# Performance work log

Measured on AMD Instinct MI355X. Metric: run time of the kernel, lower is better.

## Reference

```python
import jax, jax.numpy as jnp
import numpy as np

NN_SIZE = 10  # __init__ default nn_size


def setup_inputs() -> dict:
    key = jax.random.key(0)
    k1, k2 = jax.random.split(key)
    B, N, C = 8, 4096, 3
    xyz1 = jax.random.normal(k1, (B, N, C), dtype=jnp.float32)
    # xyz2 is a small deformation of xyz1 (realistic: deformed shape, same topology)
    xyz2 = xyz1 + 0.05 * jax.random.normal(k2, (B, N, C), dtype=jnp.float32)
    return {"xyz1": xyz1, "xyz2": xyz2}


def _knn_idx(pts, k):
    # brute-force squared-euclidean KNN of pts to itself; pts: (B,N,3) -> idx (B,N,k)
    sq = jnp.sum(pts * pts, axis=-1)                             # (B,N)
    d = sq[:, :, None] - 2.0 * jnp.einsum('bnc,bmc->bnm', pts, pts) + sq[:, None, :]
    _, idx = jax.lax.top_k(-d, k)                                # smallest distances
    return idx


def _point_to_plane(xyz, idx, k):
    # gather neighbors, center, PCA normal from 10x3 SVD, signed point-to-plane dist
    B, N, C = xyz.shape
    grouped = jax.vmap(lambda p, i: p[i])(xyz, idx)              # (B,N,k,3)
    center = jnp.mean(grouped, axis=2, keepdims=True)            # (B,N,1,3)
    local = (grouped - center).reshape(B * N, k, C)              # (B*N,k,3)
    _, _, vh = jnp.linalg.svd(local, full_matrices=False)        # vh: (B*N,3,3)
    # torch V[:, :, -1] == row -1 of Vh: singular vector of smallest singular value
    normals = jax.lax.stop_gradient(vh[:, -1, :].reshape(B, N, C))
    return jnp.sum((xyz - center[:, :, 0, :]) * normals, axis=-1)  # (B,N)


def reference(xyz1, xyz2):
    idx = _knn_idx(xyz1, NN_SIZE)
    ptof1 = _point_to_plane(xyz1, idx, NN_SIZE)
    ptof2 = _point_to_plane(xyz2, idx, NN_SIZE)
    mse = lambda a, b: jnp.mean((a - b) ** 2)
    loss = mse(jnp.abs(ptof1), jnp.abs(ptof2))
    bent = jnp.maximum(ptof2 - ptof1, 0.0)
    loss = loss + 5.0 * mse(bent, jnp.zeros_like(bent))
    return loss
```

## Files before the change

kernel.cpp:

```cpp
#include <hip/hip_runtime.h>
#include <math.h>

#define BB   8
#define NN   4096
#define KK   10
#define TPB  256
#define NPTS (BB * NN)

#define GPP  16
#define PPB  (TPB / GPP)
#define BPBK (NN / PPB)
#define KNBLK (BB * BPBK)
#define TILE 512
#define CAP  48

#define SVDBLK 256
#define SBLK   256

#define LARTG_OLD 0
#define EPSV  5.9604644775390625e-8
#define UNFLV 1.1754943508222875e-38
#define TOLV (10.0 * EPSV)

static __device__ __forceinline__ double lapy2d(double x, double y) {
  double xa = fabs(x), ya = fabs(y);
  double w = fmax(xa, ya), z = fmin(xa, ya);
  if (z == 0.0) return w;
  double q = z / w;
  return w * sqrt(1.0 + q * q);
}

static __device__ __forceinline__ void lartg(double f, double g,
                                             double &c, double &s, double &r) {
#if LARTG_OLD
  if (g == 0.0) { c = 1.0; s = 0.0; r = f; }
  else if (f == 0.0) { c = 0.0; s = 1.0; r = g; }
  else {
    double d = sqrt(f * f + g * g);
    c = f / d; s = g / d; r = d;
    if (fabs(f) > fabs(g) && c < 0.0) { c = -c; s = -s; r = -r; }
  }
#else
  if (g == 0.0) { c = 1.0; s = 0.0; r = f; }
  else if (f == 0.0) { c = 0.0; s = copysign(1.0, g); r = fabs(g); }
  else {
    double d = sqrt(f * f + g * g);
    c = fabs(f) / d;
    r = copysign(d, f);
    s = g / r;
  }
#endif
}

static __device__ void las2(double f, double g, double h, double &ssmin, double &ssmax) {
  double fa = fabs(f), ga = fabs(g), ha = fabs(h);
  double fhmn = fmin(fa, ha), fhmx = fmax(fa, ha);
  if (fhmn == 0.0) {
    ssmin = 0.0;
    if (fhmx == 0.0) ssmax = ga;
    else {
      double mn = fmin(fhmx, ga), mx = fmax(fhmx, ga);
      double rr = mn / mx;
      ssmax = mx * sqrt(1.0 + rr * rr);
    }
  } else {
    if (ga < fhmx) {
      double as_ = 1.0 + fhmn / fhmx;
      double at  = (fhmx - fhmn) / fhmx;
      double au  = (ga / fhmx); au = au * au;
      double c   = 2.0 / (sqrt(as_ * as_ + au) + sqrt(at * at + au));
      ssmin = fhmn * c;
      ssmax = fhmx / c;
    } else {
      double au = fhmx / ga;
      if (au == 0.0) { ssmin = (fhmn * fhmx) / ga; ssmax = ga; }
      else {
        double as_ = 1.0 + fhmn / fhmx;
        double at  = (fhmx - fhmn) / fhmx;
        double t1 = as_ * au, t2 = at * au;
        double c = 1.0 / (sqrt(1.0 + t1 * t1) + sqrt(1.0 + t2 * t2));
        ssmin = (fhmn * c) * au; ssmin = ssmin + ssmin;
        ssmax = ga / (c + c);
      }
    }
  }
}

static __device__ void lasv2(double f, double g, double h,
                             double &ssmin, double &ssmax,
                             double &snr, double &csr, double &snl, double &csl) {
  double ft = f, fa = fabs(f), ht = h, ha = fabs(h);
  int pmax = 1;
  bool swp = (ha > fa);
  if (swp) { pmax = 3; double t = ft; ft = ht; ht = t; t = fa; fa = ha; ha = t; }
  double gt = g, ga = fabs(g);
  double clt = 0, crt = 0, slt = 0, srt = 0;
  if (ga == 0.0) {
    ssmin = ha; ssmax = fa;
    clt = 1.0; crt = 1.0; slt = 0.0; srt = 0.0;
  } else {
    bool gasmal = true;
    if (ga > fa) {
      pmax = 2;
      if ((fa / ga) < EPSV) {
        gasmal = false;
        ssmax = ga;
        if (ha > 1.0) ssmin = fa / (ga / ha);
        else          ssmin = (fa / ga) * ha;
        clt = 1.0; slt = ht / gt; srt = 1.0; crt = ft / gt;
      }
    }
    if (gasmal) {
      double dd = fa - ha, l;
      if (dd == fa) l = 1.0; else l = dd / fa;
      double mv = gt / ft;
      double t = 2.0 - l;
      double mm = mv * mv, tt = t * t;
      double s = sqrt(tt + mm);
      double r = (l == 0.0) ? fabs(mv) : sqrt(l * l + mm);
      double a = 0.5 * (s + r);
      ssmin = ha / a;
      ssmax = fa * a;
      if (mm == 0.0) {
        if (l == 0.0) t = copysign(2.0, ft) * copysign(1.0, gt);
        else          t = gt / copysign(dd, ft) + mv / t;
      } else {
        t = (mv / (s + t) + mv / (r + l)) * (1.0 + a);
      }
      double lq = sqrt(t * t + 4.0);
      crt = 2.0 / lq;
      srt = t / lq;
      clt = (crt + srt * mv) / a;
      slt = (ht / ft) * srt / a;
    }
  }
  if (swp) { csl = srt; snl = crt; csr = slt; snr = clt; }
  else     { csl = clt; snl = slt; csr = crt; snr = srt; }
  double tsign = 1.0;
  if (pmax == 1) tsign = copysign(1.0, csr) * copysign(1.0, csl) * copysign(1.0, f);
  if (pmax == 2) tsign = copysign(1.0, snr) * copysign(1.0, csl) * copysign(1.0, g);
  if (pmax == 3) tsign = copysign(1.0, snr) * copysign(1.0, snl) * copysign(1.0, h);
  ssmax = copysign(ssmax, tsign);
  ssmin = copysign(ssmin, tsign * copysign(1.0, f) * copysign(1.0, h));
}

static __device__ __forceinline__ void rot_rows(double vt[3][3], int lo, double c, double s) {
  if (c != 1.0 || s != 0.0) {
    for (int k = 0; k < 3; ++k) {
      double tp = vt[lo + 1][k];
      vt[lo + 1][k] = c * tp - s * vt[lo][k];
      vt[lo][k]     = s * tp + c * vt[lo][k];
    }
  }
}

static __device__ void bdsqr3(double d[3], double e[2], double vt[3][3]) {
  const double tol = TOLV;
  double sminoa = fabs(d[0]);
  if (sminoa != 0.0) {
    double mu = sminoa;
    mu = fabs(d[1]) * (mu / (mu + fabs(e[0])));
    sminoa = fmin(sminoa, mu);
    if (sminoa != 0.0) {
      mu = fabs(d[2]) * (mu / (mu + fabs(e[1])));
      sminoa = fmin(sminoa, mu);
    }
  }
  sminoa /= sqrt(3.0);
  double thresh = fmax(tol * sminoa, 54.0 * UNFLV);
  int m = 3, oldll = -1, oldm = -1, idir = 0;
  double sminl = 0.0;
  for (int guard = 0; guard < 500 && m > 1; ++guard) {
    double smax = fabs(d[m - 1]);
    int ll = 0;
    bool split = false;
    for (int lll = 1; lll <= m - 1; ++lll) {
      int l = m - lll;
      double abss = fabs(d[l - 1]);
      double abse = fabs(e[l - 1]);
      if (abse <= thresh) { ll = l; split = true; break; }
      smax = fmax(smax, fmax(abss, abse));
    }
    if (split) {
      e[ll - 1] = 0.0;
      if (ll == m - 1) { m = m - 1; continue; }
      ll = ll + 1;
    } else ll = 1;
    if (ll == m - 1) {
      double sigmn, sigmx, sinr, cosr, sinl, cosl;
      lasv2(d[m - 2], e[m - 2], d[m - 1], sigmn, sigmx, sinr, cosr, sinl, cosl);
      d[m - 2] = sigmx; e[m - 2] = 0.0; d[m - 1] = sigmn;
      for (int k = 0; k < 3; ++k) {
        double x = vt[m - 2][k], y = vt[m - 1][k];
        vt[m - 2][k] = cosr * x + sinr * y;
        vt[m - 1][k] = cosr * y - sinr * x;
      }
      m -= 2;
      continue;
    }
    if (ll > oldm || m < oldll)
      idir = (fabs(d[ll - 1]) >= fabs(d[m - 1])) ? 1 : 2;
    bool deflated = false;
    if (idir == 1) {
      if (fabs(e[m - 2]) <= tol * fabs(d[m - 1])) { e[m - 2] = 0.0; continue; }
      double mu = fabs(d[ll - 1]);
      sminl = mu;
      for (int lll = ll; lll <= m - 1; ++lll) {
        if (fabs(e[lll - 1]) <= tol * mu) { e[lll - 1] = 0.0; deflated = true; break; }
        mu = fabs(d[lll]) * (mu / (mu + fabs(e[lll - 1])));
        sminl = fmin(sminl, mu);
      }
    } else {
      if (fabs(e[ll - 1]) <= tol * fabs(d[ll - 1])) { e[ll - 1] = 0.0; continue; }
      double mu = fabs(d[m - 1]);
      sminl = mu;
      for (int lll = m - 1; lll >= ll; --lll) {
        if (fabs(e[lll - 1]) <= tol * mu) { e[lll - 1] = 0.0; deflated = true; break; }
        mu = fabs(d[lll - 1]) * (mu / (mu + fabs(e[lll - 1])));
        sminl = fmin(sminl, mu);
      }
    }
    if (deflated) continue;
    oldll = ll; oldm = m;
    double shift = 0.0, rdum = 0.0;
    if (!(3.0 * tol * (sminl / smax) <= fmax(EPSV, 0.01 * tol))) {
      double sll;
      if (idir == 1) { sll = fabs(d[ll - 1]); las2(d[m - 2], e[m - 2], d[m - 1], shift, rdum); }
      else           { sll = fabs(d[m - 1]); las2(d[ll - 1], e[ll - 1], d[ll], shift, rdum); }
      if (sll > 0.0 && (shift / sll) * (shift / sll) < EPSV) shift = 0.0;
    }
    double csv[2], snv[2];
    if (shift == 0.0) {
      if (idir == 1) {
        double cs = 1.0, oldcs = 1.0, sn = 0.0, oldsn = 0.0, r = 0.0;
        for (int i = ll; i <= m - 1; ++i) {
          lartg(d[i - 1] * cs, e[i - 1], cs, sn, r);
          if (i > ll) e[i - 2] = oldsn * r;
          lartg(oldcs * r, d[i] * sn, oldcs, oldsn, d[i - 1]);
          csv[i - ll] = cs; snv[i - ll] = sn;
        }
        double h = d[m - 1] * cs;
        d[m - 1] = h * oldcs;
        e[m - 2] = h * oldsn;
        for (int j = 0; j <= m - ll - 1; ++j) rot_rows(vt, ll - 1 + j, csv[j], snv[j]);
        if (fabs(e[m - 2]) <= thresh) e[m - 2] = 0.0;
      } else {
        double cs = 1.0, oldcs = 1.0, sn = 0.0, oldsn = 0.0, r = 0.0;
        for (int i = m; i >= ll + 1; --i) {
          lartg(d[i - 1] * cs, e[i - 2], cs, sn, r);
          if (i < m) e[i - 1] = oldsn * r;
          lartg(oldcs * r, d[i - 2] * sn, oldcs, oldsn, d[i - 1]);
          csv[i - ll - 1] = oldcs; snv[i - ll - 1] = -oldsn;
        }
        double h = d[ll - 1] * cs;
        d[ll - 1] = h * oldcs;
        e[ll - 1] = h * oldsn;
        for (int j = m - ll - 1; j >= 0; --j) rot_rows(vt, ll - 1 + j, csv[j], snv[j]);
        if (fabs(e[ll - 1]) <= thresh) e[ll - 1] = 0.0;
      }
    } else {
      if (idir == 1) {
        double f = (fabs(d[ll - 1]) - shift) * (copysign(1.0, d[ll - 1]) + shift / d[ll - 1]);
        double g = e[ll - 1], cosr, sinr, cosl, sinl, r;
        for (int i = ll; i <= m - 1; ++i) {
          lartg(f, g, cosr, sinr, r);
          if (i > ll) e[i - 2] = r;
          f = cosr * d[i - 1] + sinr * e[i - 1];
          e[i - 1] = cosr * e[i - 1] - sinr * d[i - 1];
          g = sinr * d[i];
          d[i] = cosr * d[i];
          lartg(f, g, cosl, sinl, r);
          d[i - 1] = r;
          f = cosl * e[i - 1] + sinl * d[i];
          d[i] = cosl * d[i] - sinl * e[i - 1];
          if (i < m - 1) { g = sinl * e[i]; e[i] = cosl * e[i]; }
          csv[i - ll] = cosr; snv[i - ll] = sinr;
        }
        e[m - 2] = f;
        for (int j = 0; j <= m - ll - 1; ++j) rot_rows(vt, ll - 1 + j, csv[j], snv[j]);
        if (fabs(e[m - 2]) <= thresh) e[m - 2] = 0.0;
      } else {
        double f = (fabs(d[m - 1]) - shift) * (copysign(1.0, d[m - 1]) + shift / d[m - 1]);
        double g = e[m - 2], cosr, sinr, cosl, sinl, r;
        for (int i = m; i >= ll + 1; --i) {
          lartg(f, g, cosr, sinr, r);
          if (i < m) e[i - 1] = r;
          f = cosr * d[i - 1] + sinr * e[i - 2];
          e[i - 2] = cosr * e[i - 2] - sinr * d[i - 1];
          g = sinr * d[i - 2];
          d[i - 2] = cosr * d[i - 2];
          lartg(f, g, cosl, sinl, r);
          d[i - 1] = r;
          f = cosl * e[i - 2] + sinl * d[i - 2];
          d[i - 2] = cosl * d[i - 2] - sinl * e[i - 2];
          if (i > ll + 1) { g = sinl * e[i - 3]; e[i - 3] = cosl * e[i - 3]; }
          csv[i - ll - 1] = cosr; snv[i - ll - 1] = sinr;
        }
        e[ll - 1] = f;
        for (int j = m - ll - 1; j >= 0; --j) rot_rows(vt, ll - 1 + j, csv[j], snv[j]);
        if (fabs(e[ll - 1]) <= thresh) e[ll - 1] = 0.0;
      }
    }
  }
  for (int i = 0; i < 3; ++i)
    if (d[i] < 0.0) { d[i] = -d[i]; for (int k = 0; k < 3; ++k) vt[i][k] = -vt[i][k]; }
}

static __device__ void lapack_normal(double A[KK][3], double &nx, double &ny, double &nz) {
#pragma unroll
  for (int i = 0; i < 3; ++i) {
    double ss = 0.0;
#pragma unroll
    for (int j = i + 1; j < KK; ++j) ss += A[j][i] * A[j][i];
    double xnorm = sqrt(ss);
    if (xnorm != 0.0) {
      double alpha = A[i][i];
      double beta = -copysign(lapy2d(alpha, xnorm), alpha);
      double tau = (beta - alpha) / beta;
      double sc = 1.0 / (alpha - beta);
#pragma unroll
      for (int j = i + 1; j < KK; ++j) A[j][i] *= sc;
      A[i][i] = beta;
#pragma unroll
      for (int c = i + 1; c < 3; ++c) {
        double w = A[i][c];
#pragma unroll
        for (int j = i + 1; j < KK; ++j) w += A[j][i] * A[j][c];
        w *= tau;
        A[i][c] -= w;
#pragma unroll
        for (int j = i + 1; j < KK; ++j) A[j][c] -= w * A[j][i];
      }
    }
  }
  double r11 = A[0][0], r12 = A[0][1], r13 = A[0][2];
  double r22 = A[1][1], r23 = A[1][2], r33 = A[2][2];
  double d[3], e[2];
  double taup1 = 0.0, v3 = 0.0;
  d[0] = r11;
  double a22 = r22, a23 = r23, a32 = 0.0, a33 = r33;
  if (r13 != 0.0) {
    double betap = -copysign(lapy2d(r12, r13), r12);
    taup1 = (betap - r12) / betap;
    v3 = r13 / (r12 - betap);
    e[0] = betap;
    double w2 = (a22 + a23 * v3) * taup1;
    a22 -= w2; a23 -= w2 * v3;
    double w3 = (a33 * v3) * taup1;
    a32 = -w3; a33 -= w3 * v3;
  } else {
    e[0] = r12;
  }
  if (a32 != 0.0) {
    double beta2 = -copysign(lapy2d(a22, a32), a22);
    double tq = (beta2 - a22) / beta2;
    double v2 = a32 / (a22 - beta2);
    d[1] = beta2;
    double w = (a23 + v2 * a33) * tq;
    a23 -= w; a33 -= w * v2;
  } else d[1] = a22;
  e[1] = a23;
  d[2] = a33;
  double vt[3][3] = {{1,0,0},{0,1,0},{0,0,1}};
  bdsqr3(d, e, vt);
  int im = 0;
  if (d[1] < d[im]) im = 1;
  if (d[2] < d[im]) im = 2;
  double w1 = vt[im][0], w2 = vt[im][1], w3 = vt[im][2];
  double sdot = (w2 + w3 * v3) * taup1;
  w2 -= sdot; w3 -= sdot * v3;
  double inv = 1.0 / sqrt(w1 * w1 + w2 * w2 + w3 * w3);
  nx = w1 * inv; ny = w2 * inv; nz = w3 * inv;
}

#define INS2(Kp) { bool lt_ = x < Kp; unsigned long long old_ = Kp; Kp = lt_ ? x : Kp; x = lt_ ? old_ : x; }
#define CSWAPU(U,V) { if (V < U) { unsigned long long t_ = U; U = V; V = t_; } }
#define CSWAPF(U,V) { float mn_ = fminf(U, V); V = fmaxf(U, V); U = mn_; }

static __device__ __forceinline__ float dist_dd(float qx, float qy, float qz, float qw,
                                                float xi, float yi, float zi, float sqi) {
  float dot = fmaf(xi, qx, fmaf(yi, qy, __fmul_rn(zi, qz)));
  return fmaf(-2.0f, dot, __fadd_rn(sqi, qw));
}
static __device__ __forceinline__ float sqnorm(float x, float y, float z) {
  return __fadd_rn(__fadd_rn(__fmul_rn(x, x), __fmul_rn(y, y)), __fmul_rn(z, z));
}

__global__ __launch_bounds__(TPB, 1)
void lfl_knn(const float* __restrict__ xyz1, int* __restrict__ idxbuf) {
  __shared__ float4 tile[TILE];
  __shared__ unsigned long long gbuf[PPB][CAP];
  __shared__ unsigned int gcnt[PPB];
  const int t    = threadIdx.x;
  const int b    = blockIdx.x / BPBK;
  const int pb   = blockIdx.x % BPBK;
  const int g    = t >> 4;
  const int sub  = t & 15;
  const int i    = pb * PPB + g;
  const float* base = xyz1 + (size_t)b * NN * 3;

  const float xi  = base[3 * i], yi = base[3 * i + 1], zi = base[3 * i + 2];
  const float sqi = sqnorm(xi, yi, zi);

  float b0 = INFINITY, b1 = INFINITY, b2 = INFINITY, b3 = INFINITY,
        b4 = INFINITY, b5 = INFINITY, b6 = INFINITY, b7 = INFINITY;

  for (int t0 = 0; t0 < NN; t0 += TILE) {
    for (int p = t; p < TILE; p += TPB) {
      int j = t0 + p;
      float x = base[3 * j], y = base[3 * j + 1], z = base[3 * j + 2];
      tile[p] = make_float4(x, y, z, sqnorm(x, y, z));
    }
    __syncthreads();
    for (int k = 0; k < TILE / GPP; k += 8) {
      float4 q0 = tile[sub + (k + 0) * GPP];
      float4 q1 = tile[sub + (k + 1) * GPP];
      float4 q2 = tile[sub + (k + 2) * GPP];
      float4 q3 = tile[sub + (k + 3) * GPP];
      float4 q4 = tile[sub + (k + 4) * GPP];
      float4 q5 = tile[sub + (k + 5) * GPP];
      float4 q6 = tile[sub + (k + 6) * GPP];
      float4 q7 = tile[sub + (k + 7) * GPP];
      b0 = fminf(b0, dist_dd(q0.x, q0.y, q0.z, q0.w, xi, yi, zi, sqi));
      b1 = fminf(b1, dist_dd(q1.x, q1.y, q1.z, q1.w, xi, yi, zi, sqi));
      b2 = fminf(b2, dist_dd(q2.x, q2.y, q2.z, q2.w, xi, yi, zi, sqi));
      b3 = fminf(b3, dist_dd(q3.x, q3.y, q3.z, q3.w, xi, yi, zi, sqi));
      b4 = fminf(b4, dist_dd(q4.x, q4.y, q4.z, q4.w, xi, yi, zi, sqi));
      b5 = fminf(b5, dist_dd(q5.x, q5.y, q5.z, q5.w, xi, yi, zi, sqi));
      b6 = fminf(b6, dist_dd(q6.x, q6.y, q6.z, q6.w, xi, yi, zi, sqi));
      b7 = fminf(b7, dist_dd(q7.x, q7.y, q7.z, q7.w, xi, yi, zi, sqi));
    }
    __syncthreads();
  }
  CSWAPF(b0, b1) CSWAPF(b2, b3) CSWAPF(b4, b5) CSWAPF(b6, b7)
  CSWAPF(b0, b2) CSWAPF(b1, b3) CSWAPF(b4, b6) CSWAPF(b5, b7)
  CSWAPF(b1, b2) CSWAPF(b5, b6)
  CSWAPF(b0, b4) CSWAPF(b1, b5) CSWAPF(b2, b6) CSWAPF(b3, b7)
  CSWAPF(b2, b4) CSWAPF(b3, b5)
  CSWAPF(b1, b2) CSWAPF(b3, b4) CSWAPF(b5, b6)

  float thr;
  {
    float m = b0;
#pragma unroll
    for (int r = 0; r < KK; ++r) {
      m = b0;
      m = fminf(m, __shfl_xor(m, 1));
      m = fminf(m, __shfl_xor(m, 2));
      m = fminf(m, __shfl_xor(m, 4));
      m = fminf(m, __shfl_xor(m, 8));
      if (b0 == m) { b0 = b1; b1 = b2; b2 = b3; b3 = b4; b4 = b5; b5 = b6; b6 = b7; b7 = INFINITY; }
    }
    thr = m;
  }

  if (sub == 0) gcnt[g] = 0;
  __syncthreads();

  for (int t0 = 0; t0 < NN; t0 += TILE) {
    for (int p = t; p < TILE; p += TPB) {
      int j = t0 + p;
      float x = base[3 * j], y = base[3 * j + 1], z = base[3 * j + 2];
      tile[p] = make_float4(x, y, z, sqnorm(x, y, z));
    }
    __syncthreads();
#pragma unroll 8
    for (int c = sub; c < TILE; c += GPP) {
      float4 q = tile[c];
      float dd = dist_dd(q.x, q.y, q.z, q.w, xi, yi, zi, sqi);
      if (dd <= thr) {
        unsigned u = __float_as_uint(dd);
        u = (u & 0x80000000u) ? ~u : (u | 0x80000000u);
        unsigned long long key = ((unsigned long long)u << 32) | (unsigned)(t0 + c);
        unsigned pos = atomicAdd(&gcnt[g], 1u);
        if (pos < (unsigned)CAP) gbuf[g][pos] = key;
      }
    }
    __syncthreads();
  }

  const unsigned cnt = gcnt[g];
  const int gid = b * NN + i;

  if (cnt <= (unsigned)CAP) {
    unsigned long long e0 = (sub      < (int)cnt) ? gbuf[g][sub]      : ~0ULL;
    unsigned long long e1 = (sub + 16 < (int)cnt) ? gbuf[g][sub + 16] : ~0ULL;
    unsigned long long e2 = (sub + 32 < (int)cnt) ? gbuf[g][sub + 32] : ~0ULL;
    CSWAPU(e0, e1) CSWAPU(e1, e2) CSWAPU(e0, e1)
#pragma unroll
    for (int r = 0; r < KK; ++r) {
      unsigned long long m = e0, o;
      o = __shfl_xor(m, 1); m = (o < m) ? o : m;
      o = __shfl_xor(m, 2); m = (o < m) ? o : m;
      o = __shfl_xor(m, 4); m = (o < m) ? o : m;
      o = __shfl_xor(m, 8); m = (o < m) ? o : m;
      if (e0 == m) { e0 = e1; e1 = e2; e2 = ~0ULL; }
      if (sub == (r & 15)) idxbuf[gid * KK + r] = (int)(unsigned)(m & 0xFFFFFFFFULL);
    }
  } else {
    unsigned long long k0 = ~0ULL, k1 = ~0ULL, k2 = ~0ULL, k3 = ~0ULL, k4 = ~0ULL,
                       k5 = ~0ULL, k6 = ~0ULL, k7 = ~0ULL, k8 = ~0ULL, k9 = ~0ULL;
    for (int c = sub; c < NN; c += GPP) {
      float x = base[3 * c], y = base[3 * c + 1], z = base[3 * c + 2];
      float dd = dist_dd(x, y, z, sqnorm(x, y, z), xi, yi, zi, sqi);
      unsigned u = __float_as_uint(dd);
      u = (u & 0x80000000u) ? ~u : (u | 0x80000000u);
      unsigned long long key = ((unsigned long long)u << 32) | (unsigned)c;
      if (key < k9) {
        unsigned long long x2 = key;
        { unsigned long long &x = x2;
          INS2(k0) INS2(k1) INS2(k2) INS2(k3) INS2(k4)
          INS2(k5) INS2(k6) INS2(k7) INS2(k8) INS2(k9) }
      }
    }
#pragma unroll
    for (int r = 0; r < KK; ++r) {
      unsigned long long m = k0, o;
      o = __shfl_xor(m, 1); m = (o < m) ? o : m;
      o = __shfl_xor(m, 2); m = (o < m) ? o : m;
      o = __shfl_xor(m, 4); m = (o < m) ? o : m;
      o = __shfl_xor(m, 8); m = (o < m) ? o : m;
      if (k0 == m) { k0=k1;k1=k2;k2=k3;k3=k4;k4=k5;k5=k6;k6=k7;k7=k8;k8=k9;k9=~0ULL; }
      if (sub == (r & 15)) idxbuf[gid * KK + r] = (int)(unsigned)(m & 0xFFFFFFFFULL);
    }
  }
}

__global__ __launch_bounds__(TPB, 1)
void lfl_svd(const float* __restrict__ xyz1, const float* __restrict__ xyz2,
             const int* __restrict__ idxbuf, double* __restrict__ partials) {
  __shared__ double pv[TPB];
  __shared__ double red1[128], red2[128];
  const int t = threadIdx.x;
  const int half = t >> 7;
  const int lt = t & 127;
  const int pid = blockIdx.x * 128 + lt;
  const int b = pid / NN, i = pid % NN;
  const float* basep = (half == 0) ? (xyz1 + (size_t)b * NN * 3)
                                   : (xyz2 + (size_t)b * NN * 3);
  double p;
  {
    double A[KK][3];
    double cx = 0, cy = 0, cz = 0;
#pragma unroll
    for (int s = 0; s < KK; ++s) {
      int j = idxbuf[pid * KK + s];
      j = ((unsigned)j < (unsigned)NN) ? j : 0;
      A[s][0] = (double)basep[3 * j];
      A[s][1] = (double)basep[3 * j + 1];
      A[s][2] = (double)basep[3 * j + 2];
      cx += A[s][0]; cy += A[s][1]; cz += A[s][2];
    }
    cx *= 0.1; cy *= 0.1; cz *= 0.1;
#pragma unroll
    for (int s = 0; s < KK; ++s) { A[s][0] -= cx; A[s][1] -= cy; A[s][2] -= cz; }
    double nx, ny, nz;
    lapack_normal(A, nx, ny, nz);
    p = ((double)basep[3 * i] - cx) * nx + ((double)basep[3 * i + 1] - cy) * ny +
        ((double)basep[3 * i + 2] - cz) * nz;
  }
  pv[t] = p;
  __syncthreads();

  if (t < 128) {
    double p1 = pv[t], p2 = pv[t + 128];
    double da = fabs(p1) - fabs(p2);
    double df = p2 - p1;
    double bent = df > 0.0 ? df : 0.0;
    red1[t] = da * da;
    red2[t] = bent * bent;
  }
  __syncthreads();
  for (int s = 64; s > 0; s >>= 1) {
    if (t < s) { red1[t] += red1[t + s]; red2[t] += red2[t + s]; }
    __syncthreads();
  }
  if (t == 0) {
    partials[2 * blockIdx.x]     = red1[0];
    partials[2 * blockIdx.x + 1] = red2[0];
  }
}

__global__ __launch_bounds__(TPB)
void lfl_final(const double* __restrict__ partials, float* __restrict__ out) {
  __shared__ double r1[TPB], r2[TPB];
  const int t = threadIdx.x;
  r1[t] = partials[2 * t];
  r2[t] = partials[2 * t + 1];
  __syncthreads();
  for (int s = TPB / 2; s > 0; s >>= 1) {
    if (t < s) { r1[t] += r1[t + s]; r2[t] += r2[t + s]; }
    __syncthreads();
  }
  if (t == 0) out[0] = (float)((r1[0] + 5.0 * r2[0]) / (double)NPTS);
}

extern "C" void kernel_launch(void* const* d_in, const int* in_sizes, int n_in,
                              void* d_out, int out_size, void* d_ws, size_t ws_size,
                              hipStream_t stream) {
  const float* xyz1 = (const float*)d_in[0];
  const float* xyz2 = (const float*)d_in[1];
  float* out = (float*)d_out;
  double* partials = (double*)d_ws;
  int* idxbuf = (int*)((char*)d_ws + 4096);

  lfl_knn<<<KNBLK, TPB, 0, stream>>>(xyz1, idxbuf);
  lfl_svd<<<SVDBLK, TPB, 0, stream>>>(xyz1, xyz2, idxbuf, partials);
  lfl_final<<<1, TPB, 0, stream>>>(partials, out);
}
```

Before: 108.0 us.

## Restructure KNN kernel: whole-batch LDS tile, per-thread query, slice-split candidates

The KNN kernel now loads all 4096 points of a batch into shared memory once per block, instead of reloading 512-point tiles twice. Each thread owns one query point and scans a quarter slice of the candidates, so the shared-memory reads become wave-uniform broadcasts rather than 16-lane groups striding through the tile. Per-slice top-8 minima are combined across four threads to form the threshold. Candidate capacity drops from 48 to 32, and the block grows to 512 threads with a large LDS footprint, which limits occupancy and may send more points to the brute-force fallback.

```diff
diff --git a/kernel.cpp b/kernel.cpp
--- a/kernel.cpp
+++ b/kernel.cpp
@@ -7,12 +7,13 @@
 #define TPB  256
 #define NPTS (BB * NN)
 
-#define GPP  16
-#define PPB  (TPB / GPP)
-#define BPBK (NN / PPB)
-#define KNBLK (BB * BPBK)
-#define TILE 512
-#define CAP  48
+#define KTPB  512
+#define PTS   128
+#define NSL   4
+#define SLICE (NN / NSL)
+#define NACC  8
+#define KBLK  (NPTS / PTS)
+#define CAP2  32
 
 #define SVDBLK 256
 #define SBLK   256
@@ -386,51 +387,57 @@
   return __fadd_rn(__fadd_rn(__fmul_rn(x, x), __fmul_rn(y, y)), __fmul_rn(z, z));
 }
 
-__global__ __launch_bounds__(TPB, 1)
+__global__ __launch_bounds__(KTPB, 1)
 void lfl_knn(const float* __restrict__ xyz1, int* __restrict__ idxbuf) {
-  __shared__ float4 tile[TILE];
-  __shared__ unsigned long long gbuf[PPB][CAP];
-  __shared__ unsigned int gcnt[PPB];
+  __shared__ float4 tile[NN];
+  __shared__ unsigned long long umem[PTS * CAP2];
+  __shared__ float thrv[PTS];
+  __shared__ unsigned int gcnt[PTS];
+  float (*accs)[PTS][NACC] = (float (*)[PTS][NACC])umem;
+  unsigned long long (*gbuf)[CAP2] = (unsigned long long (*)[CAP2])umem;
+
   const int t    = threadIdx.x;
-  const int b    = blockIdx.x / BPBK;
-  const int pb   = blockIdx.x % BPBK;
-  const int g    = t >> 4;
-  const int sub  = t & 15;
-  const int i    = pb * PPB + g;
+  const int w    = t >> 6;
+  const int lane = t & 63;
+  const int half = w >> 2;
+  const int sl   = w & 3;
+  const int myp  = half * 64 + lane;
+  const int bpb  = NN / PTS;
+  const int b    = blockIdx.x / bpb;
+  const int pb   = blockIdx.x % bpb;
   const float* base = xyz1 + (size_t)b * NN * 3;
 
-  const float xi  = base[3 * i], yi = base[3 * i + 1], zi = base[3 * i + 2];
-  const float sqi = sqnorm(xi, yi, zi);
+  for (int p = t; p < NN; p += KTPB) {
+    float x = base[3 * p], y = base[3 * p + 1], z = base[3 * p + 2];
+    tile[p] = make_float4(x, y, z, sqnorm(x, y, z));
+  }
+  if (t < PTS) gcnt[t] = 0;
+  __syncthreads();
+
+  const int   ii = pb * PTS + myp;
+  const float4 qp = tile[ii];
+  const float xi = qp.x, yi = qp.y, zi = qp.z, sqi = qp.w;
+  const int   sb = sl * SLICE;
 
   float b0 = INFINITY, b1 = INFINITY, b2 = INFINITY, b3 = INFINITY,
         b4 = INFINITY, b5 = INFINITY, b6 = INFINITY, b7 = INFINITY;
-
-  for (int t0 = 0; t0 < NN; t0 += TILE) {
-    for (int p = t; p < TILE; p += TPB) {
-      int j = t0 + p;
-      float x = base[3 * j], y = base[3 * j + 1], z = base[3 * j + 2];
-      tile[p] = make_float4(x, y, z, sqnorm(x, y, z));
-    }
-    __syncthreads();
-    for (int k = 0; k < TILE / GPP; k += 8) {
-      float4 q0 = tile[sub + (k + 0) * GPP];
-      float4 q1 = tile[sub + (k + 1) * GPP];
-      float4 q2 = tile[sub + (k + 2) * GPP];
-      float4 q3 = tile[sub + (k + 3) * GPP];
-      float4 q4 = tile[sub + (k + 4) * GPP];
-      float4 q5 = tile[sub + (k + 5) * GPP];
-      float4 q6 = tile[sub + (k + 6) * GPP];
-      float4 q7 = tile[sub + (k + 7) * GPP];
-      b0 = fminf(b0, dist_dd(q0.x, q0.y, q0.z, q0.w, xi, yi, zi, sqi));
-      b1 = fminf(b1, dist_dd(q1.x, q1.y, q1.z, q1.w, xi, yi, zi, sqi));
-      b2 = fminf(b2, dist_dd(q2.x, q2.y, q2.z, q2.w, xi, yi, zi, sqi));
-      b3 = fminf(b3, dist_dd(q3.x, q3.y, q3.z, q3.w, xi, yi, zi, sqi));
-      b4 = fminf(b4, dist_dd(q4.x, q4.y, q4.z, q4.w, xi, yi, zi, sqi));
-      b5 = fminf(b5, dist_dd(q5.x, q5.y, q5.z, q5.w, xi, yi, zi, sqi));
-      b6 = fminf(b6, dist_dd(q6.x, q6.y, q6.z, q6.w, xi, yi, zi, sqi));
-      b7 = fminf(b7, dist_dd(q7.x, q7.y, q7.z, q7.w, xi, yi, zi, sqi));
-    }
-    __syncthreads();
+  for (int k = 0; k < SLICE; k += NACC) {
+    float4 q0 = tile[sb + k + 0];
+    float4 q1 = tile[sb + k + 1];
+    float4 q2 = tile[sb + k + 2];
+    float4 q3 = tile[sb + k + 3];
+    float4 q4 = tile[sb + k + 4];
+    float4 q5 = tile[sb + k + 5];
+    float4 q6 = tile[sb + k + 6];
+    float4 q7 = tile[sb + k + 7];
+    b0 = fminf(b0, dist_dd(q0.x, q0.y, q0.z, q0.w, xi, yi, zi, sqi));
+    b1 = fminf(b1, dist_dd(q1.x, q1.y, q1.z, q1.w, xi, yi, zi, sqi));
+    b2 = fminf(b2, dist_dd(q2.x, q2.y, q2.z, q2.w, xi, yi, zi, sqi));
+    b3 = fminf(b3, dist_dd(q3.x, q3.y, q3.z, q3.w, xi, yi, zi, sqi));
+    b4 = fminf(b4, dist_dd(q4.x, q4.y, q4.z, q4.w, xi, yi, zi, sqi));
+    b5 = fminf(b5, dist_dd(q5.x, q5.y, q5.z, q5.w, xi, yi, zi, sqi));
+    b6 = fminf(b6, dist_dd(q6.x, q6.y, q6.z, q6.w, xi, yi, zi, sqi));
+    b7 = fminf(b7, dist_dd(q7.x, q7.y, q7.z, q7.w, xi, yi, zi, sqi));
   }
   CSWAPF(b0, b1) CSWAPF(b2, b3) CSWAPF(b4, b5) CSWAPF(b6, b7)
   CSWAPF(b0, b2) CSWAPF(b1, b3) CSWAPF(b4, b6) CSWAPF(b5, b7)
@@ -438,90 +445,99 @@
   CSWAPF(b0, b4) CSWAPF(b1, b5) CSWAPF(b2, b6) CSWAPF(b3, b7)
   CSWAPF(b2, b4) CSWAPF(b3, b5)
   CSWAPF(b1, b2) CSWAPF(b3, b4) CSWAPF(b5, b6)
-
-  float thr;
+  accs[sl][myp][0] = b0; accs[sl][myp][1] = b1; accs[sl][myp][2] = b2; accs[sl][myp][3] = b3;
+  accs[sl][myp][4] = b4; accs[sl][myp][5] = b5; accs[sl][myp][6] = b6; accs[sl][myp][7] = b7;
+  __syncthreads();
+
   {
-    float m = b0;
+    const int pt = t >> 2, slot = t & 3;
+    float c0 = accs[slot][pt][0], c1 = accs[slot][pt][1], c2 = accs[slot][pt][2],
+          c3 = accs[slot][pt][3], c4 = accs[slot][pt][4], c5 = accs[slot][pt][5],
+          c6 = accs[slot][pt][6], c7 = accs[slot][pt][7];
+    float m = c0;
 #pragma unroll
     for (int r = 0; r < KK; ++r) {
-      m = b0;
+      m = c0;
       m = fminf(m, __shfl_xor(m, 1));
       m = fminf(m, __shfl_xor(m, 2));
-      m = fminf(m, __shfl_xor(m, 4));
-      m = fminf(m, __shfl_xor(m, 8));
-      if (b0 == m) { b0 = b1; b1 = b2; b2 = b3; b3 = b4; b4 = b5; b5 = b6; b6 = b7; b7 = INFINITY; }
-    }
-    thr = m;
-  }
-
-  if (sub == 0) gcnt[g] = 0;
+      if (c0 == m) { c0 = c1; c1 = c2; c2 = c3; c3 = c4; c4 = c5; c5 = c6; c6 = c7; c7 = INFINITY; }
+    }
+    if (slot == 0) thrv[pt] = m;
+  }
   __syncthreads();
 
-  for (int t0 = 0; t0 < NN; t0 += TILE) {
-    for (int p = t; p < TILE; p += TPB) {
-      int j = t0 + p;
-      float x = base[3 * j], y = base[3 * j + 1], z = base[3 * j + 2];
-      tile[p] = make_float4(x, y, z, sqnorm(x, y, z));
-    }
-    __syncthreads();
-#pragma unroll 8
-    for (int c = sub; c < TILE; c += GPP) {
-      float4 q = tile[c];
-      float dd = dist_dd(q.x, q.y, q.z, q.w, xi, yi, zi, sqi);
-      if (dd <= thr) {
+  {
+    const float thr = thrv[myp];
+    for (int k = 0; k < SLICE; k += NACC) {
+#pragma unroll
+      for (int r = 0; r < NACC; ++r) {
+        float4 q = tile[sb + k + r];
+        float dd = dist_dd(q.x, q.y, q.z, q.w, xi, yi, zi, sqi);
+        if (dd <= thr) {
+          unsigned u = __float_as_uint(dd);
+          u = (u & 0x80000000u) ? ~u : (u | 0x80000000u);
+          unsigned long long key = ((unsigned long long)u << 32) | (unsigned)(sb + k + r);
+          unsigned pos = atomicAdd(&gcnt[myp], 1u);
+          if (pos < (unsigned)CAP2) gbuf[myp][pos] = key;
+        }
+      }
+    }
+  }
+  __syncthreads();
+
+  {
+    const int pt = t >> 2, slot = t & 3;
+    const unsigned cnt = gcnt[pt];
+    const int pgid = b * NN + pb * PTS + pt;
+    if (cnt <= (unsigned)CAP2) {
+      unsigned long long e0 = (slot      < (int)cnt) ? gbuf[pt][slot]      : ~0ULL;
+      unsigned long long e1 = (slot + 4  < (int)cnt) ? gbuf[pt][slot + 4]  : ~0ULL;
+      unsigned long long e2 = (slot + 8  < (int)cnt) ? gbuf[pt][slot + 8]  : ~0ULL;
+      unsigned long long e3 = (slot + 12 < (int)cnt) ? gbuf[pt][slot + 12] : ~0ULL;
+      unsigned long long e4 = (slot + 16 < (int)cnt) ? gbuf[pt][slot + 16] : ~0ULL;
+      unsigned long long e5 = (slot + 20 < (int)cnt) ? gbuf[pt][slot + 20] : ~0ULL;
+      unsigned long long e6 = (slot + 24 < (int)cnt) ? gbuf[pt][slot + 24] : ~0ULL;
+      unsigned long long e7 = (slot + 28 < (int)cnt) ? gbuf[pt][slot + 28] : ~0ULL;
+      CSWAPU(e0, e1) CSWAPU(e2, e3) CSWAPU(e4, e5) CSWAPU(e6, e7)
+      CSWAPU(e0, e2) CSWAPU(e1, e3) CSWAPU(e4, e6) CSWAPU(e5, e7)
+      CSWAPU(e1, e2) CSWAPU(e5, e6)
+      CSWAPU(e0, e4) CSWAPU(e1, e5) CSWAPU(e2, e6) CSWAPU(e3, e7)
+      CSWAPU(e2, e4) CSWAPU(e3, e5)
+      CSWAPU(e1, e2) CSWAPU(e3, e4) CSWAPU(e5, e6)
+#pragma unroll
+      for (int r = 0; r < KK; ++r) {
+        unsigned long long m = e0, o;
+        o = __shfl_xor(m, 1); m = (o < m) ? o : m;
+        o = __shfl_xor(m, 2); m = (o < m) ? o : m;
+        if (e0 == m) { e0 = e1; e1 = e2; e2 = e3; e3 = e4; e4 = e5; e5 = e6; e6 = e7; e7 = ~0ULL; }
+        if (slot == (r & 3)) idxbuf[pgid * KK + r] = (int)(unsigned)(m & 0xFFFFFFFFULL);
+      }
+    } else {
+      float4 qq = tile[pb * PTS + pt];
+      float fxi = qq.x, fyi = qq.y, fzi = qq.z, fsq = qq.w;
+      unsigned long long k0 = ~0ULL, k1 = ~0ULL, k2 = ~0ULL, k3 = ~0ULL, k4 = ~0ULL,
+                         k5 = ~0ULL, k6 = ~0ULL, k7 = ~0ULL, k8 = ~0ULL, k9 = ~0ULL;
+      for (int c = slot; c < NN; c += 4) {
+        float4 q = tile[c];
+        float dd = dist_dd(q.x, q.y, q.z, q.w, fxi, fyi, fzi, fsq);
         unsigned u = __float_as_uint(dd);
         u = (u & 0x80000000u) ? ~u : (u | 0x80000000u);
-        unsigned long long key = ((unsigned long long)u << 32) | (unsigned)(t0 + c);
-        unsigned pos = atomicAdd(&gcnt[g], 1u);
-        if (pos < (unsigned)CAP) gbuf[g][pos] = key;
-      }
-    }
-    __syncthreads();
-  }
-
-  const unsigned cnt = gcnt[g];
-  const int gid = b * NN + i;
-
-  if (cnt <= (unsigned)CAP) {
-    unsigned long long e0 = (sub      < (int)cnt) ? gbuf[g][sub]      : ~0ULL;
-    unsigned long long e1 = (sub + 16 < (int)cnt) ? gbuf[g][sub + 16] : ~0ULL;
-    unsigned long long e2 = (sub + 32 < (int)cnt) ? gbuf[g][sub + 32] : ~0ULL;
-    CSWAPU(e0, e1) CSWAPU(e1, e2) CSWAPU(e0, e1)
-#pragma unroll
-    for (int r = 0; r < KK; ++r) {
-      unsigned long long m = e0, o;
-      o = __shfl_xor(m, 1); m = (o < m) ? o : m;
-      o = __shfl_xor(m, 2); m = (o < m) ? o : m;
-      o = __shfl_xor(m, 4); m = (o < m) ? o : m;
-      o = __shfl_xor(m, 8); m = (o < m) ? o : m;
-      if (e0 == m) { e0 = e1; e1 = e2; e2 = ~0ULL; }
-      if (sub == (r & 15)) idxbuf[gid * KK + r] = (int)(unsigned)(m & 0xFFFFFFFFULL);
-    }
-  } else {
-    unsigned long long k0 = ~0ULL, k1 = ~0ULL, k2 = ~0ULL, k3 = ~0ULL, k4 = ~0ULL,
-                       k5 = ~0ULL, k6 = ~0ULL, k7 = ~0ULL, k8 = ~0ULL, k9 = ~0ULL;
-    for (int c = sub; c < NN; c += GPP) {
-      float x = base[3 * c], y = base[3 * c + 1], z = base[3 * c + 2];
-      float dd = dist_dd(x, y, z, sqnorm(x, y, z), xi, yi, zi, sqi);
-      unsigned u = __float_as_uint(dd);
-      u = (u & 0x80000000u) ? ~u : (u | 0x80000000u);
-      unsigned long long key = ((unsigned long long)u << 32) | (unsigned)c;
-      if (key < k9) {
-        unsigned long long x2 = key;
-        { unsigned long long &x = x2;
-          INS2(k0) INS2(k1) INS2(k2) INS2(k3) INS2(k4)
-          INS2(k5) INS2(k6) INS2(k7) INS2(k8) INS2(k9) }
-      }
-    }
-#pragma unroll
-    for (int r = 0; r < KK; ++r) {
-      unsigned long long m = k0, o;
-      o = __shfl_xor(m, 1); m = (o < m) ? o : m;
-      o = __shfl_xor(m, 2); m = (o < m) ? o : m;
-      o = __shfl_xor(m, 4); m = (o < m) ? o : m;
-      o = __shfl_xor(m, 8); m = (o < m) ? o : m;
-      if (k0 == m) { k0=k1;k1=k2;k2=k3;k3=k4;k4=k5;k5=k6;k6=k7;k7=k8;k8=k9;k9=~0ULL; }
-      if (sub == (r & 15)) idxbuf[gid * KK + r] = (int)(unsigned)(m & 0xFFFFFFFFULL);
+        unsigned long long key = ((unsigned long long)u << 32) | (unsigned)c;
+        if (key < k9) {
+          unsigned long long x2 = key;
+          { unsigned long long &x = x2;
+            INS2(k0) INS2(k1) INS2(k2) INS2(k3) INS2(k4)
+            INS2(k5) INS2(k6) INS2(k7) INS2(k8) INS2(k9) }
+        }
+      }
+#pragma unroll
+      for (int r = 0; r < KK; ++r) {
+        unsigned long long m = k0, o;
+        o = __shfl_xor(m, 1); m = (o < m) ? o : m;
+        o = __shfl_xor(m, 2); m = (o < m) ? o : m;
+        if (k0 == m) { k0=k1;k1=k2;k2=k3;k3=k4;k4=k5;k5=k6;k6=k7;k7=k8;k8=k9;k9=~0ULL; }
+        if (slot == (r & 3)) idxbuf[pgid * KK + r] = (int)(unsigned)(m & 0xFFFFFFFFULL);
+      }
     }
   }
 }
@@ -604,7 +620,7 @@
   double* partials = (double*)d_ws;
   int* idxbuf = (int*)((char*)d_ws + 4096);
 
-  lfl_knn<<<KNBLK, TPB, 0, stream>>>(xyz1, idxbuf);
+  lfl_knn<<<KBLK, KTPB, 0, stream>>>(xyz1, idxbuf);
   lfl_svd<<<SVDBLK, TPB, 0, stream>>>(xyz1, xyz2, idxbuf, partials);
   lfl_final<<<1, TPB, 0, stream>>>(partials, out);
 }
```

Result: slower. 148.2 us (+37.2%).
